# Kernel tuning notes

Hardware: AMD Instinct MI355X
Metric: run time of the kernel (lower is better)

Reference implementation:

```python
import jax, jax.numpy as jnp
import numpy as np

D_MODEL = 1024
NHEAD = 16
EPS = 1e-5


def layer_norm(x, scale, bias):
    mu = jnp.mean(x, axis=-1, keepdims=True)
    var = jnp.var(x, axis=-1, keepdims=True)
    return (x - mu) * jax.lax.rsqrt(var + EPS) * scale + bias


def setup_inputs() -> dict:
    key = jax.random.key(0)
    ks = jax.random.split(key, 8)
    B, S, D = 4, 2048, D_MODEL
    s = 1.0 / np.sqrt(D)
    return {
        "x": jax.random.normal(ks[0], (B, S, D), dtype=jnp.float32),
        "Wq": jax.random.normal(ks[1], (D, D), dtype=jnp.float32) * s,
        "Wk": jax.random.normal(ks[2], (D, D), dtype=jnp.float32) * s,
        "Wv": jax.random.normal(ks[3], (D, D), dtype=jnp.float32) * s,
        "W1": jax.random.normal(ks[4], (D, D), dtype=jnp.float32) * s,
        "b1": jnp.zeros((D,), dtype=jnp.float32),
        "W2": jax.random.normal(ks[5], (D, D), dtype=jnp.float32) * s,
        "b2": jnp.zeros((D,), dtype=jnp.float32),
        "ln1_scale": jnp.ones((D,), dtype=jnp.float32),
        "ln1_bias": jnp.zeros((D,), dtype=jnp.float32),
        "ln2_scale": jnp.ones((D,), dtype=jnp.float32),
        "ln2_bias": jnp.zeros((D,), dtype=jnp.float32),
    }


def reference(x, Wq, Wk, Wv, W1, b1, W2, b2, ln1_scale, ln1_bias, ln2_scale, ln2_bias):
    B, S, D = x.shape
    H = NHEAD
    dh = D // H
    x = layer_norm(x, ln1_scale, ln1_bias)
    # torch Linear: y = x @ W.T (no bias for q/k/v)
    q = jnp.einsum('bsd,ed->bse', x, Wq).reshape(B, S, H, dh).transpose(0, 2, 1, 3)
    k = jnp.einsum('bsd,ed->bse', x, Wk).reshape(B, S, H, dh).transpose(0, 2, 1, 3)
    v = jnp.einsum('bsd,ed->bse', x, Wv).reshape(B, S, H, dh).transpose(0, 2, 1, 3)
    # NOTE: original module applies NO 1/sqrt(dh) scaling — kept faithful.
    scores = jnp.einsum('bhqd,bhkd->bhqk', q, k)
    attn = jax.nn.softmax(scores, axis=-1)  # dropout is identity in eval
    att = jnp.einsum('bhqk,bhkd->bhqd', attn, v)
    att = att.transpose(0, 2, 1, 3).reshape(B, S, D)
    xt = layer_norm(x + att, ln2_scale, ln2_bias)
    h = jax.nn.relu(jnp.einsum('bsd,ed->bse', xt, W1) + b1)
    ffn = jnp.einsum('bsd,ed->bse', h, W2) + b2
    return xt + ffn
```

## Files before the change

kernel.cpp:

```cpp
#include <hip/hip_runtime.h>
#include <stdint.h>

typedef unsigned short u16;
typedef __attribute__((ext_vector_type(4))) float f32x4;
typedef _Float16 h16;
typedef __attribute__((ext_vector_type(8))) _Float16 f16x8;
typedef __attribute__((ext_vector_type(4))) _Float16 h16x4;
typedef __attribute__((ext_vector_type(2))) __fp16 fp16v2;

#define DMODEL 1024
#define SEQ    2048
#define BATCH  4
#define NHEAD  16
#define DH     64
#define NTOK   (BATCH*SEQ)
#define BH     (BATCH*NHEAD)
#define EPS    1e-5f
#define LOG2E  1.44269504f

__device__ __forceinline__ void gload_lds16(const void* g, void* l){
  __builtin_amdgcn_global_load_lds((__attribute__((address_space(1))) unsigned int*)g,
                                   (__attribute__((address_space(3))) unsigned int*)l,
                                   16, 0, 0);
}

__device__ __forceinline__ int swzkey(int row){ return (row&7) ^ ((row>>3)&7); }

__global__ __launch_bounds__(256) void prep_weights(const float* __restrict__ Wq,
                                                    const float* __restrict__ Wk,
                                                    const float* __restrict__ Wv,
                                                    const float* __restrict__ W1,
                                                    const float* __restrict__ W2,
                                                    h16* __restrict__ wqkv,
                                                    h16* __restrict__ w1h,
                                                    h16* __restrict__ w2h){
  const int nW = DMODEL*DMODEL;
  int r = blockIdx.x >> 10;
  int i = ((blockIdx.x & 1023)*256 + threadIdx.x)*4;
  const float* src = (r==0) ? Wq : (r==1) ? Wk : (r==2) ? Wv : (r==3) ? W1 : W2;
  h16* dst = (r==0) ? wqkv : (r==1) ? (wqkv+nW) : (r==2) ? (wqkv+2*nW) : (r==3) ? w1h : w2h;
  float4 v = *reinterpret_cast<const float4*>(src + i);
  h16x4 o; o[0]=(h16)v.x; o[1]=(h16)v.y; o[2]=(h16)v.z; o[3]=(h16)v.w;
  *reinterpret_cast<h16x4*>(dst + i) = o;
}

__global__ __launch_bounds__(256) void ln_kernel(const float* __restrict__ in0,
                                                 const float* __restrict__ sc,
                                                 const float* __restrict__ bi,
                                                 float* __restrict__ of32,
                                                 h16* __restrict__ oh16){
  int row = blockIdx.x*4 + (threadIdx.x>>6);
  int l = threadIdx.x & 63;
  size_t rbase = (size_t)row*DMODEL;
  float v[16];
  #pragma unroll
  for (int q=0;q<4;++q){
    float4 t = *reinterpret_cast<const float4*>(in0 + rbase + q*256 + l*4);
    v[q*4]=t.x; v[q*4+1]=t.y; v[q*4+2]=t.z; v[q*4+3]=t.w;
  }
  float s=0.f, ss=0.f;
  #pragma unroll
  for (int j=0;j<16;++j){ s += v[j]; ss += v[j]*v[j]; }
  #pragma unroll
  for (int m=1;m<64;m<<=1){ s += __shfl_xor(s,m); ss += __shfl_xor(ss,m); }
  float mu  = s * (1.0f/DMODEL);
  float var = fmaxf(ss * (1.0f/DMODEL) - mu*mu, 0.0f);
  float r = rsqrtf(var + EPS);
  #pragma unroll
  for (int q=0;q<4;++q){
    float4 g = *reinterpret_cast<const float4*>(sc + q*256 + l*4);
    float4 b = *reinterpret_cast<const float4*>(bi + q*256 + l*4);
    float o0 = (v[q*4  ]-mu)*r*g.x + b.x;
    float o1 = (v[q*4+1]-mu)*r*g.y + b.y;
    float o2 = (v[q*4+2]-mu)*r*g.z + b.z;
    float o3 = (v[q*4+3]-mu)*r*g.w + b.w;
    size_t off = rbase + q*256 + l*4;
    if (of32){
      float4 ov; ov.x=o0; ov.y=o1; ov.z=o2; ov.w=o3;
      *reinterpret_cast<float4*>(of32 + off) = ov;
    }
    if (oh16){
      h16x4 oh; oh[0]=(h16)o0; oh[1]=(h16)o1; oh[2]=(h16)o2; oh[3]=(h16)o3;
      *reinterpret_cast<h16x4*>(oh16 + off) = oh;
    }
  }
}

__global__ __launch_bounds__(256) void gemm_qkv(const h16* __restrict__ xn,
                                                const h16* __restrict__ wqkv,
                                                h16* __restrict__ qT,
                                                h16* __restrict__ kR,
                                                h16* __restrict__ vT){
  const int K = DMODEL;
  __shared__ h16 As[128*64], Bs[128*64];
  int t = threadIdx.x, l = t&63, w = t>>6;
  int bm = blockIdx.y, bn = blockIdx.x;
  int wr = w>>1, wc = w&1;
  const h16* Bsrc = wqkv + (size_t)bn*128*K;

  f32x4 acc[4][4];
  #pragma unroll
  for (int m=0;m<4;++m)
    #pragma unroll
    for (int n=0;n<4;++n)
      #pragma unroll
      for (int i=0;i<4;++i) acc[m][n][i] = 0.0f;

  const int nk = K/64;
  for (int kt=0; kt<nk; ++kt){
    int k0 = kt*64;
    __syncthreads();
    #pragma unroll
    for (int i=0;i<4;++i){
      int slot = i*256 + t;
      int row = slot>>3, pc = slot&7;
      int lc = pc ^ swzkey(row);
      gload_lds16(xn + (size_t)(bm*128 + row)*K + k0 + lc*8, &As[slot*8]);
      gload_lds16(Bsrc + (size_t)row*K + k0 + lc*8, &Bs[slot*8]);
    }
    __syncthreads();
    #pragma unroll
    for (int ks=0; ks<2; ++ks){
      f16x8 af[4], bf[4];
      #pragma unroll
      for (int m=0;m<4;++m){
        int row = wr*64 + m*16 + (l&15);
        int cp = (ks*4 + (l>>4)) ^ swzkey(row);
        af[m] = *reinterpret_cast<const f16x8*>(&As[row*64 + cp*8]);
      }
      #pragma unroll
      for (int n=0;n<4;++n){
        int row = wc*64 + n*16 + (l&15);
        int cp = (ks*4 + (l>>4)) ^ swzkey(row);
        bf[n] = *reinterpret_cast<const f16x8*>(&Bs[row*64 + cp*8]);
      }
      __builtin_amdgcn_s_setprio(1);
      #pragma unroll
      for (int m=0;m<4;++m)
        #pragma unroll
        for (int n=0;n<4;++n)
          acc[m][n] = __builtin_amdgcn_mfma_f32_16x16x32_f16(af[m], bf[n], acc[m][n], 0,0,0);
      __builtin_amdgcn_s_setprio(0);
    }
  }

  const bool isK = (bn >= 8 && bn < 16);
  const bool isQ = (bn < 8);
  #pragma unroll
  for (int m=0;m<4;++m){
    int row0 = bm*128 + wr*64 + m*16 + ((l>>4)<<2);
    int b = row0 >> 11, s0 = row0 & 2047;
    #pragma unroll
    for (int n=0;n<4;++n){
      int col = bn*128 + wc*64 + n*16 + (l&15);
      int dg = col & 1023;
      int hh = dg >> 6, dh = dg & 63;
      if (isK){
        #pragma unroll
        for (int i=0;i<4;++i)
          kR[((size_t)(b*NHEAD + hh)*SEQ + s0 + i)*DH + dh] = (h16)acc[m][n][i];
      } else {
        h16x4 ov;
        #pragma unroll
        for (int i=0;i<4;++i){
          float vv = acc[m][n][i];
          if (isQ) vv *= LOG2E;
          ov[i] = (h16)vv;
        }
        int s0p = isQ ? s0 : ((s0 & ~31) + (((s0>>2)&3)<<3) + (((s0>>4)&1)<<2));
        h16* dst = (isQ ? qT : vT) + ((size_t)(b*NHEAD + hh)*DH + dh)*SEQ + s0p;
        *reinterpret_cast<h16x4*>(dst) = ov;
      }
    }
  }
}

template<bool RELU, bool RES, bool OUTF32>
__global__ __launch_bounds__(256) void gemm_ffn(const h16* __restrict__ A,
                                                const h16* __restrict__ W,
                                                const float* __restrict__ bias,
                                                const float* __restrict__ resid,
                                                void* __restrict__ outp,
                                                int M, int N, int K){
  __shared__ h16 As[128*64];
  __shared__ h16 Bs[128*64];
  int t = threadIdx.x, l = t&63, w = t>>6;
  int bm = blockIdx.y, bn = blockIdx.x;
  int wr = w>>1, wc = w&1;
  f32x4 acc[4][4];
  #pragma unroll
  for (int m=0;m<4;++m)
    #pragma unroll
    for (int n=0;n<4;++n)
      #pragma unroll
      for (int i=0;i<4;++i) acc[m][n][i] = 0.0f;

  const int nk = K/64;
  for (int kt=0; kt<nk; ++kt){
    int k0 = kt*64;
    __syncthreads();
    #pragma unroll
    for (int i=0;i<4;++i){
      int slot = i*256 + t;
      int row = slot>>3, pc = slot&7;
      int lc = pc ^ swzkey(row);
      gload_lds16(A + (size_t)(bm*128 + row)*K + k0 + lc*8, &As[slot*8]);
      gload_lds16(W + (size_t)(bn*128 + row)*K + k0 + lc*8, &Bs[slot*8]);
    }
    __syncthreads();
    #pragma unroll
    for (int ks=0; ks<2; ++ks){
      f16x8 af[4], bf[4];
      #pragma unroll
      for (int m=0;m<4;++m){
        int row = wr*64 + m*16 + (l&15);
        int cp = (ks*4 + (l>>4)) ^ swzkey(row);
        af[m] = *reinterpret_cast<const f16x8*>(&As[row*64 + cp*8]);
      }
      #pragma unroll
      for (int n=0;n<4;++n){
        int row = wc*64 + n*16 + (l&15);
        int cp = (ks*4 + (l>>4)) ^ swzkey(row);
        bf[n] = *reinterpret_cast<const f16x8*>(&Bs[row*64 + cp*8]);
      }
      __builtin_amdgcn_s_setprio(1);
      #pragma unroll
      for (int m=0;m<4;++m)
        #pragma unroll
        for (int n=0;n<4;++n)
          acc[m][n] = __builtin_amdgcn_mfma_f32_16x16x32_f16(af[m], bf[n], acc[m][n], 0,0,0);
      __builtin_amdgcn_s_setprio(0);
    }
  }

  #pragma unroll
  for (int m=0;m<4;++m){
    int row0 = bm*128 + wr*64 + m*16 + ((l>>4)<<2);
    #pragma unroll
    for (int n=0;n<4;++n){
      int col = bn*128 + wc*64 + n*16 + (l&15);
      float bv = bias[col];
      #pragma unroll
      for (int i=0;i<4;++i){
        float vv = acc[m][n][i] + bv;
        if (RELU) vv = fmaxf(vv, 0.0f);
        size_t off = (size_t)(row0+i)*N + col;
        if (RES) vv += resid[off];
        if (OUTF32) ((float*)outp)[off] = vv;
        else        ((h16*)outp)[off] = (h16)vv;
      }
    }
  }
}

#define QBLK 256
#define KBLK 64
#define RESC_THR_L2 11.5415603f
#define NROWS (BH*8*256)

__global__ __launch_bounds__(512, 2) void attn_split(const h16* __restrict__ qT,
                                                     const h16* __restrict__ kR,
                                                     const h16* __restrict__ vT,
                                                     h16* __restrict__ outP0,
                                                     h16* __restrict__ outP1,
                                                     float2* __restrict__ lm){
  int id = blockIdx.x;
  int bh   = (id & 7) + ((id >> 7) << 3);
  int qb   = (id >> 3) & 7;
  int half = (id >> 6) & 1;
  int t = threadIdx.x, l = t&63, w = t>>6;
  int g = l>>4;

  const size_t hbase = (size_t)bh * SEQ * DH;
  const h16* khb = kR + hbase + (size_t)half*(SEQ/2)*DH;
  const h16* qtb = qT + hbase;
  const h16* vtb = vT + hbase + half*(SEQ/2);
  int q0 = qb*QBLK + w*32;

  f16x8 qf[2][2];
  #pragma unroll
  for (int qs=0;qs<2;++qs)
    #pragma unroll
    for (int kc=0;kc<2;++kc)
      #pragma unroll
      for (int j=0;j<8;++j)
        qf[qs][kc][j] = qtb[(size_t)(kc*32 + g*8 + j)*SEQ + q0 + qs*16 + (l&15)];

  __shared__ h16 Kh2[2][KBLK*64];
  __shared__ h16 Vt2[2][KBLK*64];

  int offs[8];
  #pragma unroll
  for (int kc=0;kc<2;++kc)
    #pragma unroll
    for (int st=0;st<4;++st){
      int rr = st*16 + (l&15);
      offs[kc*4+st] = rr*128 + (((kc*4 + g) ^ swzkey(rr))<<4);
    }

  int srow = t>>3, spc = t&7;
  int slc = spc ^ swzkey(srow);
  const h16* ksrc = khb + (size_t)srow*DH + slc*8;
  const h16* vsrc = vtb + (size_t)srow*SEQ + slc*8;

  f32x4 o[2][4];
  #pragma unroll
  for (int qs=0;qs<2;++qs)
    #pragma unroll
    for (int dt=0;dt<4;++dt)
      #pragma unroll
      for (int i=0;i<4;++i) o[qs][dt][i] = 0.0f;
  float m_run[2] = {-3.0e38f, -3.0e38f};
  float l_run[2] = {0.0f, 0.0f};

  const fp16v2 one2 = {(__fp16)1.0f, (__fp16)1.0f};

  #define STAGE(bb)                                  \
    { gload_lds16(ksrc, &Kh2[bb][t*8]);              \
      gload_lds16(vsrc, &Vt2[bb][t*8]);              \
      ksrc += KBLK*DH; vsrc += KBLK; }

  STAGE(0);
  int cur = 0;
  const int NT = SEQ/2/KBLK;
  for (int kt=0; kt<NT; ++kt){
    __syncthreads();
    if (kt+1 < NT) STAGE(cur^1);

    char* KhB = (char*)&Kh2[cur][0];
    char* VtB = (char*)&Vt2[cur][0];

    f32x4 sc[2][4];
    #pragma unroll
    for (int qs=0;qs<2;++qs)
      #pragma unroll
      for (int st=0;st<4;++st)
        #pragma unroll
        for (int i=0;i<4;++i) sc[qs][st][i] = 0.0f;

    #pragma unroll
    for (int kc=0;kc<2;++kc)
      #pragma unroll
      for (int st=0;st<4;++st){
        f16x8 kf = *reinterpret_cast<const f16x8*>(KhB + offs[kc*4+st]);
        __builtin_amdgcn_s_setprio(1);
        sc[0][st] = __builtin_amdgcn_mfma_f32_16x16x32_f16(kf, qf[0][kc], sc[0][st], 0,0,0);
        sc[1][st] = __builtin_amdgcn_mfma_f32_16x16x32_f16(kf, qf[1][kc], sc[1][st], 0,0,0);
        __builtin_amdgcn_s_setprio(0);
      }

    float mt[2];
    #pragma unroll
    for (int qs=0;qs<2;++qs){
      const float* s = (const float*)&sc[qs][0];
      float m0 = fmaxf(s[0], s[1]);
      #pragma unroll
      for (int j=2;j<16;j+=2) m0 = fmaxf(fmaxf(m0, s[j]), s[j+1]);
      m0 = fmaxf(m0, __shfl_xor(m0, 16));
      m0 = fmaxf(m0, __shfl_xor(m0, 32));
      mt[qs] = m0;
    }
    bool defer = (__all((mt[0] <= m_run[0] + RESC_THR_L2) &&
                        (mt[1] <= m_run[1] + RESC_THR_L2)) != 0);

    union { unsigned u[4]; f16x8 v; } pfu[2][2];
    #pragma unroll
    for (int qs=0;qs<2;++qs){
      float mn = defer ? m_run[qs] : fmaxf(m_run[qs], mt[qs]);
      const float* s = (const float*)&sc[qs][0];
      float psum = 0.0f;
      #pragma unroll
      for (int kc=0;kc<2;++kc)
        #pragma unroll
        for (int j=0;j<4;++j){
          float p0 = exp2f(s[kc*8+2*j]   - mn);
          float p1 = exp2f(s[kc*8+2*j+1] - mn);
          union { fp16v2 v2; unsigned u; } c;
          c.v2 = __builtin_amdgcn_cvt_pkrtz(p0, p1);
          pfu[qs][kc].u[j] = c.u;
#if __has_builtin(__builtin_amdgcn_fdot2)
          psum = __builtin_amdgcn_fdot2(c.v2, one2, psum, false);
#else
          psum += p0 + p1;
#endif
        }
      if (defer){
        l_run[qs] += psum;
      } else {
        float scl = exp2f(m_run[qs] - mn);
        m_run[qs] = mn;
        l_run[qs] = l_run[qs]*scl + psum;
        #pragma unroll
        for (int dt=0;dt<4;++dt)
          #pragma unroll
          for (int i=0;i<4;++i) o[qs][dt][i] *= scl;
      }
    }

    #pragma unroll
    for (int kc=0;kc<2;++kc)
      #pragma unroll
      for (int dt=0;dt<4;++dt){
        f16x8 vf = *reinterpret_cast<const f16x8*>(VtB + offs[kc*4+dt]);
        __builtin_amdgcn_s_setprio(1);
        o[0][dt] = __builtin_amdgcn_mfma_f32_16x16x32_f16(vf, pfu[0][kc].v, o[0][dt], 0,0,0);
        o[1][dt] = __builtin_amdgcn_mfma_f32_16x16x32_f16(vf, pfu[1][kc].v, o[1][dt], 0,0,0);
        __builtin_amdgcn_s_setprio(0);
      }
    cur ^= 1;
  }

  h16* outP = half ? outP1 : outP0;
  int rowbase = (bh*8 + qb)*256 + w*32;
  #pragma unroll
  for (int qs=0;qs<2;++qs){
    float lt = l_run[qs];
    lt += __shfl_xor(lt, 16);
    lt += __shfl_xor(lt, 32);
    float inv = 1.0f / lt;
    int row = rowbase + qs*16 + (l&15);
    #pragma unroll
    for (int dt=0;dt<4;++dt){
      h16x4 ov;
      #pragma unroll
      for (int i=0;i<4;++i) ov[i] = (h16)(o[qs][dt][i] * inv);
      *reinterpret_cast<h16x4*>(outP + (size_t)row*64 + dt*16 + (g<<2)) = ov;
    }
    if (l < 16)
      lm[half*NROWS + row] = make_float2(m_run[qs], lt);
  }
}

__global__ __launch_bounds__(256) void ln2_combine(const float* __restrict__ xn,
                                                   const h16* __restrict__ p0,
                                                   const h16* __restrict__ p1,
                                                   const float2* __restrict__ lm,
                                                   const float* __restrict__ sc,
                                                   const float* __restrict__ bi,
                                                   float* __restrict__ of32,
                                                   h16* __restrict__ oh16){
  int token = blockIdx.x*4 + (threadIdx.x>>6);
  int l = threadIdx.x & 63;
  int b = token >> 11, qb = (token >> 8) & 7, r = token & 255;
  int hh = l >> 2;
  int rowg = ((b*NHEAD + hh)*8 + qb)*256 + r;
  float2 A = lm[rowg];
  float2 B = lm[NROWS + rowg];
  float ms = fmaxf(A.x, B.x);
  float w0 = A.y * exp2f(A.x - ms);
  float w1 = B.y * exp2f(B.x - ms);
  float inv = 1.0f / (w0 + w1);
  w0 *= inv; w1 *= inv;

  const f16x8* q0 = reinterpret_cast<const f16x8*>(p0 + (size_t)rowg*64 + (l&3)*16);
  const f16x8* q1 = reinterpret_cast<const f16x8*>(p1 + (size_t)rowg*64 + (l&3)*16);
  size_t base = (size_t)token*DMODEL + l*16;
  float v[16];
  #pragma unroll
  for (int c=0;c<2;++c){
    f16x8 a = q0[c], bb = q1[c];
    #pragma unroll
    for (int j=0;j<8;++j)
      v[c*8+j] = (float)a[j]*w0 + (float)bb[j]*w1;
  }
  #pragma unroll
  for (int q=0;q<4;++q){
    float4 t = *reinterpret_cast<const float4*>(xn + base + q*4);
    v[q*4] += t.x; v[q*4+1] += t.y; v[q*4+2] += t.z; v[q*4+3] += t.w;
  }

  float s=0.f, ss=0.f;
  #pragma unroll
  for (int j=0;j<16;++j){ s += v[j]; ss += v[j]*v[j]; }
  #pragma unroll
  for (int m=1;m<64;m<<=1){ s += __shfl_xor(s,m); ss += __shfl_xor(ss,m); }
  float mu  = s * (1.0f/DMODEL);
  float var = fmaxf(ss * (1.0f/DMODEL) - mu*mu, 0.0f);
  float rr = rsqrtf(var + EPS);
  #pragma unroll
  for (int q=0;q<4;++q){
    float4 g = *reinterpret_cast<const float4*>(sc + l*16 + q*4);
    float4 bb = *reinterpret_cast<const float4*>(bi + l*16 + q*4);
    float o0 = (v[q*4  ]-mu)*rr*g.x + bb.x;
    float o1 = (v[q*4+1]-mu)*rr*g.y + bb.y;
    float o2 = (v[q*4+2]-mu)*rr*g.z + bb.z;
    float o3 = (v[q*4+3]-mu)*rr*g.w + bb.w;
    float4 ov; ov.x=o0; ov.y=o1; ov.z=o2; ov.w=o3;
    *reinterpret_cast<float4*>(of32 + base + q*4) = ov;
    h16x4 oh; oh[0]=(h16)o0; oh[1]=(h16)o1; oh[2]=(h16)o2; oh[3]=(h16)o3;
    *reinterpret_cast<h16x4*>(oh16 + base + q*4) = oh;
  }
}

extern "C" void kernel_launch(void* const* d_in, const int* in_sizes, int n_in,
                              void* d_out, int out_size, void* d_ws, size_t ws_size,
                              hipStream_t stream){
  (void)in_sizes; (void)n_in; (void)out_size; (void)ws_size;
  const float* x    = (const float*)d_in[0];
  const float* Wq   = (const float*)d_in[1];
  const float* Wk   = (const float*)d_in[2];
  const float* Wv   = (const float*)d_in[3];
  const float* W1   = (const float*)d_in[4];
  const float* b1   = (const float*)d_in[5];
  const float* W2   = (const float*)d_in[6];
  const float* b2   = (const float*)d_in[7];
  const float* ln1s = (const float*)d_in[8];
  const float* ln1b = (const float*)d_in[9];
  const float* ln2s = (const float*)d_in[10];
  const float* ln2b = (const float*)d_in[11];

  char* ws = (char*)d_ws;
  float* xn_f32  = (float*)ws;  ws += (size_t)NTOK*DMODEL*4;
  h16* part0     = (h16*)ws;    ws += (size_t)NTOK*DMODEL*2;
  h16* part1     = (h16*)ws;    ws += (size_t)NTOK*DMODEL*2;
  float* xt_f32  = (float*)ws;  ws += (size_t)NTOK*DMODEL*4;
  h16* xn_h      = (h16*)ws;    ws += (size_t)NTOK*DMODEL*2;
  h16* qT_h      = (h16*)ws;    ws += (size_t)NTOK*DMODEL*2;
  h16* k_h       = (h16*)ws;    ws += (size_t)NTOK*DMODEL*2;
  h16* vT_h      = (h16*)ws;    ws += (size_t)NTOK*DMODEL*2;
  h16* xt_h      = (h16*)ws;    ws += (size_t)NTOK*DMODEL*2;
  h16* h_h       = (h16*)ws;    ws += (size_t)NTOK*DMODEL*2;
  h16* wqkv_h    = (h16*)ws;    ws += (size_t)3*DMODEL*DMODEL*2;
  h16* w1h       = (h16*)ws;    ws += (size_t)DMODEL*DMODEL*2;
  h16* w2h       = (h16*)ws;    ws += (size_t)DMODEL*DMODEL*2;
  float2* lm     = (float2*)ws; ws += (size_t)2*NROWS*8;

  prep_weights<<<5120, 256, 0, stream>>>(Wq, Wk, Wv, W1, W2, wqkv_h, w1h, w2h);

  ln_kernel<<<NTOK/4, 256, 0, stream>>>(x, ln1s, ln1b, xn_f32, xn_h);

  gemm_qkv<<<dim3(3*DMODEL/128, NTOK/128), 256, 0, stream>>>(
      xn_h, wqkv_h, qT_h, k_h, vT_h);

  attn_split<<<BH*(SEQ/QBLK)*2, 512, 0, stream>>>(qT_h, k_h, vT_h, part0, part1, lm);

  ln2_combine<<<NTOK/4, 256, 0, stream>>>(xn_f32, part0, part1, lm,
                                          ln2s, ln2b, xt_f32, xt_h);

  gemm_ffn<true,false,false><<<dim3(DMODEL/128, NTOK/128), 256, 0, stream>>>(
      xt_h, w1h, b1, nullptr, h_h, NTOK, DMODEL, DMODEL);

  gemm_ffn<false,true,true><<<dim3(DMODEL/128, NTOK/128), 256, 0, stream>>>(
      h_h, w2h, b2, xt_f32, d_out, NTOK, DMODEL, DMODEL);
}
```

Measured before the change: 309.7 us.

## Remap GEMM blocks per XCD, compute softmax row sums via MFMA, use native exp2

The GEMM kernels now launch on a 1D grid and remap block IDs so that each XCD handles a contiguous band of row tiles, which should improve L2 reuse of A tiles. The attention kernel drops the per-element fdot2 row-sum and accumulates the softmax denominator with an extra MFMA against a ones matrix. It also moves the cross-lane max shuffles inside the non-deferred rescale branch, and uses the hardware exp2 builtin in place of exp2f. The added MFMAs increase matrix-core work slightly, the lane-local max test for defer changes the rescale criterion, and the native exp2 may differ slightly in accuracy.

```diff
diff --git a/kernel.cpp b/kernel.cpp
--- a/kernel.cpp
+++ b/kernel.cpp
@@ -22,6 +22,14 @@
   __builtin_amdgcn_global_load_lds((__attribute__((address_space(1))) unsigned int*)g,
                                    (__attribute__((address_space(3))) unsigned int*)l,
                                    16, 0, 0);
+}
+
+__device__ __forceinline__ float fastexp2(float x){
+#if __has_builtin(__builtin_amdgcn_exp2f)
+  return __builtin_amdgcn_exp2f(x);
+#else
+  return exp2f(x);
+#endif
 }
 
 __device__ __forceinline__ int swzkey(int row){ return (row&7) ^ ((row>>3)&7); }
@@ -93,8 +101,11 @@
                                                 h16* __restrict__ vT){
   const int K = DMODEL;
   __shared__ h16 As[128*64], Bs[128*64];
+  int id = blockIdx.x;
+  int xcd = id & 7, j = id >> 3;
+  int bm = xcd*8 + j/24;
+  int bn = j - (j/24)*24;
   int t = threadIdx.x, l = t&63, w = t>>6;
-  int bm = blockIdx.y, bn = blockIdx.x;
   int wr = w>>1, wc = w&1;
   const h16* Bsrc = wqkv + (size_t)bn*128*K;
 
@@ -184,8 +195,12 @@
                                                 int M, int N, int K){
   __shared__ h16 As[128*64];
   __shared__ h16 Bs[128*64];
+  int id = blockIdx.x;
+  int xcd = id & 7, j = id >> 3;
+  int nbn = N >> 7;
+  int bm = xcd*((M>>7)>>3) + j/nbn;
+  int bn = j - (j/nbn)*nbn;
   int t = threadIdx.x, l = t&63, w = t>>6;
-  int bm = blockIdx.y, bn = blockIdx.x;
   int wr = w>>1, wc = w&1;
   f32x4 acc[4][4];
   #pragma unroll
@@ -310,10 +325,16 @@
     for (int dt=0;dt<4;++dt)
       #pragma unroll
       for (int i=0;i<4;++i) o[qs][dt][i] = 0.0f;
+  f32x4 lacc[2];
+  #pragma unroll
+  for (int qs=0;qs<2;++qs)
+    #pragma unroll
+    for (int i=0;i<4;++i) lacc[qs][i] = 0.0f;
   float m_run[2] = {-3.0e38f, -3.0e38f};
-  float l_run[2] = {0.0f, 0.0f};
-
-  const fp16v2 one2 = {(__fp16)1.0f, (__fp16)1.0f};
+
+  f16x8 onesA;
+  #pragma unroll
+  for (int j=0;j<8;++j) onesA[j] = (h16)1.0f;
 
   #define STAGE(bb)                                  \
     { gload_lds16(ksrc, &Kh2[bb][t*8]);              \
@@ -349,56 +370,58 @@
         __builtin_amdgcn_s_setprio(0);
       }
 
-    float mt[2];
+    float lmax[2];
     #pragma unroll
     for (int qs=0;qs<2;++qs){
       const float* s = (const float*)&sc[qs][0];
       float m0 = fmaxf(s[0], s[1]);
       #pragma unroll
       for (int j=2;j<16;j+=2) m0 = fmaxf(fmaxf(m0, s[j]), s[j+1]);
-      m0 = fmaxf(m0, __shfl_xor(m0, 16));
-      m0 = fmaxf(m0, __shfl_xor(m0, 32));
-      mt[qs] = m0;
-    }
-    bool defer = (__all((mt[0] <= m_run[0] + RESC_THR_L2) &&
-                        (mt[1] <= m_run[1] + RESC_THR_L2)) != 0);
+      lmax[qs] = m0;
+    }
+    bool defer = (__all((lmax[0] <= m_run[0] + RESC_THR_L2) &&
+                        (lmax[1] <= m_run[1] + RESC_THR_L2)) != 0);
+    if (!defer){
+      #pragma unroll
+      for (int qs=0;qs<2;++qs){
+        float m0 = lmax[qs];
+        m0 = fmaxf(m0, __shfl_xor(m0, 16));
+        m0 = fmaxf(m0, __shfl_xor(m0, 32));
+        float mn = fmaxf(m_run[qs], m0);
+        float scl = fastexp2(m_run[qs] - mn);
+        m_run[qs] = mn;
+        #pragma unroll
+        for (int dt=0;dt<4;++dt)
+          #pragma unroll
+          for (int i=0;i<4;++i) o[qs][dt][i] *= scl;
+        #pragma unroll
+        for (int i=0;i<4;++i) lacc[qs][i] *= scl;
+      }
+    }
 
     union { unsigned u[4]; f16x8 v; } pfu[2][2];
     #pragma unroll
     for (int qs=0;qs<2;++qs){
-      float mn = defer ? m_run[qs] : fmaxf(m_run[qs], mt[qs]);
+      float mn = m_run[qs];
       const float* s = (const float*)&sc[qs][0];
-      float psum = 0.0f;
       #pragma unroll
       for (int kc=0;kc<2;++kc)
         #pragma unroll
         for (int j=0;j<4;++j){
-          float p0 = exp2f(s[kc*8+2*j]   - mn);
-          float p1 = exp2f(s[kc*8+2*j+1] - mn);
+          float p0 = fastexp2(s[kc*8+2*j]   - mn);
+          float p1 = fastexp2(s[kc*8+2*j+1] - mn);
           union { fp16v2 v2; unsigned u; } c;
           c.v2 = __builtin_amdgcn_cvt_pkrtz(p0, p1);
           pfu[qs][kc].u[j] = c.u;
-#if __has_builtin(__builtin_amdgcn_fdot2)
-          psum = __builtin_amdgcn_fdot2(c.v2, one2, psum, false);
-#else
-          psum += p0 + p1;
-#endif
         }
-      if (defer){
-        l_run[qs] += psum;
-      } else {
-        float scl = exp2f(m_run[qs] - mn);
-        m_run[qs] = mn;
-        l_run[qs] = l_run[qs]*scl + psum;
-        #pragma unroll
-        for (int dt=0;dt<4;++dt)
-          #pragma unroll
-          for (int i=0;i<4;++i) o[qs][dt][i] *= scl;
-      }
-    }
-
-    #pragma unroll
-    for (int kc=0;kc<2;++kc)
+    }
+
+    #pragma unroll
+    for (int kc=0;kc<2;++kc){
+      __builtin_amdgcn_s_setprio(1);
+      lacc[0] = __builtin_amdgcn_mfma_f32_16x16x32_f16(onesA, pfu[0][kc].v, lacc[0], 0,0,0);
+      lacc[1] = __builtin_amdgcn_mfma_f32_16x16x32_f16(onesA, pfu[1][kc].v, lacc[1], 0,0,0);
+      __builtin_amdgcn_s_setprio(0);
       #pragma unroll
       for (int dt=0;dt<4;++dt){
         f16x8 vf = *reinterpret_cast<const f16x8*>(VtB + offs[kc*4+dt]);
@@ -407,6 +430,7 @@
         o[1][dt] = __builtin_amdgcn_mfma_f32_16x16x32_f16(vf, pfu[1][kc].v, o[1][dt], 0,0,0);
         __builtin_amdgcn_s_setprio(0);
       }
+    }
     cur ^= 1;
   }
 
@@ -414,9 +438,7 @@
   int rowbase = (bh*8 + qb)*256 + w*32;
   #pragma unroll
   for (int qs=0;qs<2;++qs){
-    float lt = l_run[qs];
-    lt += __shfl_xor(lt, 16);
-    lt += __shfl_xor(lt, 32);
+    float lt = lacc[qs][0];
     float inv = 1.0f / lt;
     int row = rowbase + qs*16 + (l&15);
     #pragma unroll
@@ -447,8 +469,8 @@
   float2 A = lm[rowg];
   float2 B = lm[NROWS + rowg];
   float ms = fmaxf(A.x, B.x);
-  float w0 = A.y * exp2f(A.x - ms);
-  float w1 = B.y * exp2f(B.x - ms);
+  float w0 = A.y * fastexp2(A.x - ms);
+  float w1 = B.y * fastexp2(B.x - ms);
   float inv = 1.0f / (w0 + w1);
   w0 *= inv; w1 *= inv;
 
@@ -529,7 +551,7 @@
 
   ln_kernel<<<NTOK/4, 256, 0, stream>>>(x, ln1s, ln1b, xn_f32, xn_h);
 
-  gemm_qkv<<<dim3(3*DMODEL/128, NTOK/128), 256, 0, stream>>>(
+  gemm_qkv<<<3*DMODEL/128 * (NTOK/128), 256, 0, stream>>>(
       xn_h, wqkv_h, qT_h, k_h, vT_h);
 
   attn_split<<<BH*(SEQ/QBLK)*2, 512, 0, stream>>>(qT_h, k_h, vT_h, part0, part1, lm);
@@ -537,9 +559,9 @@
   ln2_combine<<<NTOK/4, 256, 0, stream>>>(xn_f32, part0, part1, lm,
                                           ln2s, ln2b, xt_f32, xt_h);
 
-  gemm_ffn<true,false,false><<<dim3(DMODEL/128, NTOK/128), 256, 0, stream>>>(
+  gemm_ffn<true,false,false><<<(DMODEL/128) * (NTOK/128), 256, 0, stream>>>(
       xt_h, w1h, b1, nullptr, h_h, NTOK, DMODEL, DMODEL);
 
-  gemm_ffn<false,true,true><<<dim3(DMODEL/128, NTOK/128), 256, 0, stream>>>(
+  gemm_ffn<false,true,true><<<(DMODEL/128) * (NTOK/128), 256, 0, stream>>>(
       h_h, w2h, b2, xt_f32, d_out, NTOK, DMODEL, DMODEL);
 }
```

Result: faster. 273.6 us (-11.6%).
